# Optimization experiments

Measured on AMD Instinct MI355X. Metric: run time of the kernel, lower is better.

Reference implementation:

```python
import jax, jax.numpy as jnp
import numpy as np

R = 512   # rnn_size
K = 2     # context_size (number of memories in queue)


def _lstm_cell(x, h, c, Wih, Whh, bih, bhh):
    # PyTorch LSTMCell: gates ordered i, f, g, o
    gates = x @ Wih.T + h @ Whh.T + bih + bhh
    i, f, g, o = jnp.split(gates, 4, axis=1)
    i = jax.nn.sigmoid(i)
    f = jax.nn.sigmoid(f)
    g = jnp.tanh(g)
    o = jax.nn.sigmoid(o)
    c = f * c + i * g
    h = o * jnp.tanh(c)
    return h, c


def setup_inputs() -> dict:
    key = jax.random.key(0)
    ks = jax.random.split(key, 12)
    T, B, N = 64, 16, 256
    emb_utts = jax.random.normal(ks[0], (T, B, R), jnp.float32)
    M = jax.random.normal(ks[1], (K, B, N, R), jnp.float32)
    z = jnp.zeros((B, R), jnp.float32)
    s = 0.1  # param init scale to avoid gate saturation
    params = {
        'Wih_r': s * jax.random.normal(ks[2], (4 * R, 2 * R), jnp.float32),
        'Whh_r': s * jax.random.normal(ks[3], (4 * R, R), jnp.float32),
        'bih_r': s * jax.random.normal(ks[4], (4 * R,), jnp.float32),
        'bhh_r': s * jax.random.normal(ks[5], (4 * R,), jnp.float32),
        'Wc':    s * jax.random.normal(ks[6], (R, K * R + R), jnp.float32),
        'bc':    s * jax.random.normal(ks[7], (R,), jnp.float32),
        'Wih_w': s * jax.random.normal(ks[8], (4 * R, R), jnp.float32),
        'Whh_w': s * jax.random.normal(ks[9], (4 * R, R), jnp.float32),
        'bih_w': s * jax.random.normal(ks[10], (4 * R,), jnp.float32),
        'bhh_w': s * jax.random.normal(ks[11], (4 * R,), jnp.float32),
    }
    return dict(emb_utts=emb_utts, hr0=z, cr0=z, hw0=z, cw0=z,
                init_output=z, M=M, **params)


def reference(emb_utts, hr0, cr0, hw0, cw0, init_output, M,
              Wih_r, Whh_r, bih_r, bhh_r, Wc, bc,
              Wih_w, Whh_w, bih_w, bhh_w):
    B = emb_utts.shape[1]

    def step(carry, w):
        hr, cr, hw, cw, Mq = carry
        # input_feed: out is never updated in the original loop -> init_output
        x = jnp.concatenate([w, init_output], axis=1)
        hr, cr = _lstm_cell(x, hr, cr, Wih_r, Whh_r, bih_r, bhh_r)
        # read each memory: sim [K,B,N], z softmax over slots, m [K,B,R]
        sim = jnp.einsum('br,kbnr->kbn', hr, Mq)
        z = jax.nn.softmax(sim, axis=-1)
        m = jnp.einsum('kbn,kbnr->kbr', z, Mq)
        cattet = jnp.concatenate(
            [hr, m.transpose(1, 0, 2).reshape(B, K * R)], axis=1)
        comp = jax.nn.softmax(cattet @ Wc.T + bc, axis=-1)
        hw, cw = _lstm_cell(comp, hw, cw, Wih_w, Whh_w, bih_w, bhh_w)
        # NTM-style update: M_new = (1 - z) * (M + hw)
        erase = 1.0 - z[..., None]                    # [K,B,N,1]
        Mq = erase * (Mq + hw[None, :, None, :])      # [K,B,N,R]
        return (hr, cr, hw, cw, Mq), hw

    (hr, cr, hw, cw, Mf), outputs = jax.lax.scan(
        step, (hr0, cr0, hw0, cw0, M), emb_utts)
    return outputs, hr, cr, hw, cw, Mf
```

## Files before the change

### kernel.cpp

```cpp
#include <hip/hip_runtime.h>
#include <math.h>

#define RR 512
#define BB 16
#define TT 64
#define KC 2
#define NN 256
#define NBLK 256

__device__ __forceinline__ float sigmoidf_(float x) {
    return 1.0f / (1.0f + __expf(-x));
}
__device__ __forceinline__ float wave_sum(float v) {
    #pragma unroll
    for (int off = 32; off > 0; off >>= 1) v += __shfl_xor(v, off, 64);
    return v;
}
__device__ __forceinline__ float wave_max(float v) {
    #pragma unroll
    for (int off = 32; off > 0; off >>= 1) v = fmaxf(v, __shfl_xor(v, off, 64));
    return v;
}

__device__ __forceinline__ float ldA(const float* p) {
    return __hip_atomic_load(p, __ATOMIC_RELAXED, __HIP_MEMORY_SCOPE_AGENT);
}
__device__ __forceinline__ void stA(float* p, float v) {
    __hip_atomic_store(p, v, __ATOMIC_RELAXED, __HIP_MEMORY_SCOPE_AGENT);
}
__device__ __forceinline__ unsigned ldU(const unsigned* p) {
    return __hip_atomic_load(p, __ATOMIC_RELAXED, __HIP_MEMORY_SCOPE_AGENT);
}
__device__ __forceinline__ void stU(unsigned* p, unsigned v) {
    __hip_atomic_store(p, v, __ATOMIC_RELAXED, __HIP_MEMORY_SCOPE_AGENT);
}
__device__ __forceinline__ float2 ldA2(const float* p) {
    unsigned long long v = __hip_atomic_load((const unsigned long long*)p,
                                             __ATOMIC_RELAXED, __HIP_MEMORY_SCOPE_AGENT);
    float2 r;
    r.x = __uint_as_float((unsigned)v);
    r.y = __uint_as_float((unsigned)(v >> 32));
    return r;
}
__device__ __forceinline__ void stA2(float* p, float x, float y) {
    unsigned long long v = ((unsigned long long)__float_as_uint(y) << 32)
                         | (unsigned long long)__float_as_uint(x);
    __hip_atomic_store((unsigned long long*)p, v, __ATOMIC_RELAXED,
                       __HIP_MEMORY_SCOPE_AGENT);
}


#define LDG8(d0,d1,d2,d3,d4,d5,d6,d7, q0,q1,q2,q3,q4,q5,q6,q7)      \
    asm volatile(                                                     \
        "global_load_dwordx4 %0, %8, off sc0 sc1\n\t"                \
        "global_load_dwordx4 %1, %9, off sc0 sc1\n\t"                \
        "global_load_dwordx4 %2, %10, off sc0 sc1\n\t"               \
        "global_load_dwordx4 %3, %11, off sc0 sc1\n\t"               \
        "global_load_dwordx4 %4, %12, off sc0 sc1\n\t"               \
        "global_load_dwordx4 %5, %13, off sc0 sc1\n\t"               \
        "global_load_dwordx4 %6, %14, off sc0 sc1\n\t"               \
        "global_load_dwordx4 %7, %15, off sc0 sc1\n\t"               \
        "s_waitcnt vmcnt(0)"                                          \
        : "=&v"(d0), "=&v"(d1), "=&v"(d2), "=&v"(d3),                 \
          "=&v"(d4), "=&v"(d5), "=&v"(d6), "=&v"(d7)                  \
        : "v"(q0), "v"(q1), "v"(q2), "v"(q3),                         \
          "v"(q4), "v"(q5), "v"(q6), "v"(q7)                          \
        : "memory")

#define LDG16O(d0,d1,d2,d3,d4,d5,d6,d7,d8,d9,d10,d11,d12,d13,d14,d15,\
               q0,q1,q2,q3)                                           \
    asm volatile(                                                     \
        "global_load_dwordx4 %0, %16, off sc0 sc1\n\t"               \
        "global_load_dwordx4 %1, %16, off offset:1024 sc0 sc1\n\t"   \
        "global_load_dwordx4 %2, %16, off offset:2048 sc0 sc1\n\t"   \
        "global_load_dwordx4 %3, %16, off offset:3072 sc0 sc1\n\t"   \
        "global_load_dwordx4 %4, %17, off sc0 sc1\n\t"               \
        "global_load_dwordx4 %5, %17, off offset:1024 sc0 sc1\n\t"   \
        "global_load_dwordx4 %6, %17, off offset:2048 sc0 sc1\n\t"   \
        "global_load_dwordx4 %7, %17, off offset:3072 sc0 sc1\n\t"   \
        "global_load_dwordx4 %8, %18, off sc0 sc1\n\t"               \
        "global_load_dwordx4 %9, %18, off offset:1024 sc0 sc1\n\t"   \
        "global_load_dwordx4 %10, %18, off offset:2048 sc0 sc1\n\t"  \
        "global_load_dwordx4 %11, %18, off offset:3072 sc0 sc1\n\t"  \
        "global_load_dwordx4 %12, %19, off sc0 sc1\n\t"              \
        "global_load_dwordx4 %13, %19, off offset:1024 sc0 sc1\n\t"  \
        "global_load_dwordx4 %14, %19, off offset:2048 sc0 sc1\n\t"  \
        "global_load_dwordx4 %15, %19, off offset:3072 sc0 sc1\n\t"  \
        "s_waitcnt vmcnt(0)"                                          \
        : "=&v"(d0), "=&v"(d1), "=&v"(d2), "=&v"(d3),                 \
          "=&v"(d4), "=&v"(d5), "=&v"(d6), "=&v"(d7),                 \
          "=&v"(d8), "=&v"(d9), "=&v"(d10), "=&v"(d11),               \
          "=&v"(d12), "=&v"(d13), "=&v"(d14), "=&v"(d15)              \
        : "v"(q0), "v"(q1), "v"(q2), "v"(q3)                          \
        : "memory")

struct f8 { float4 a, b; };
__device__ __forceinline__ f8 ld8s(const float* row, int lane) {
    f8 r;
    r.a = *(const float4*)(row + lane * 4);
    r.b = *(const float4*)(row + 256 + lane * 4);
    return r;
}
__device__ __forceinline__ void st8s(float* row, const f8& v, int lane) {
    *(float4*)(row + lane * 4) = v.a;
    *(float4*)(row + 256 + lane * 4) = v.b;
}
__device__ __forceinline__ f8 ld8sA2(const float* row, int lane) {
    float2 t0 = ldA2(row + lane * 4);
    float2 t1 = ldA2(row + lane * 4 + 2);
    float2 t2 = ldA2(row + 256 + lane * 4);
    float2 t3 = ldA2(row + 256 + lane * 4 + 2);
    f8 r;
    r.a = make_float4(t0.x, t0.y, t1.x, t1.y);
    r.b = make_float4(t2.x, t2.y, t3.x, t3.y);
    return r;
}
__device__ __forceinline__ float dot8(const f8& x, const f8& y) {
    return x.a.x*y.a.x + x.a.y*y.a.y + x.a.z*y.a.z + x.a.w*y.a.w
         + x.b.x*y.b.x + x.b.y*y.b.y + x.b.z*y.b.z + x.b.w*y.b.w;
}
__device__ __forceinline__ void upd8(f8& m, const f8& u, float zf) {
    m.a.x = zf * (m.a.x + u.a.x); m.a.y = zf * (m.a.y + u.a.y);
    m.a.z = zf * (m.a.z + u.a.z); m.a.w = zf * (m.a.w + u.a.w);
    m.b.x = zf * (m.b.x + u.b.x); m.b.y = zf * (m.b.y + u.b.y);
    m.b.z = zf * (m.b.z + u.b.z); m.b.w = zf * (m.b.w + u.b.w);
}
__device__ __forceinline__ void fmaacc8(f8& acc, float sc, const f8& m, float wgt) {
    acc.a.x = acc.a.x*sc + wgt*m.a.x; acc.a.y = acc.a.y*sc + wgt*m.a.y;
    acc.a.z = acc.a.z*sc + wgt*m.a.z; acc.a.w = acc.a.w*sc + wgt*m.a.w;
    acc.b.x = acc.b.x*sc + wgt*m.b.x; acc.b.y = acc.b.y*sc + wgt*m.b.y;
    acc.b.z = acc.b.z*sc + wgt*m.b.z; acc.b.w = acc.b.w*sc + wgt*m.b.w;
}

__device__ __forceinline__ float reduce16(float* p, int lane) {
    float q[8];
    {
        bool hi = (lane & 32) != 0;
        #pragma unroll
        for (int i = 0; i < 8; ++i) {
            float snd = hi ? p[i] : p[i + 8];
            float r = __shfl_xor(snd, 32, 64);
            q[i] = (hi ? p[i + 8] : p[i]) + r;
        }
    }
    float s4[4];
    {
        bool hi = (lane & 16) != 0;
        #pragma unroll
        for (int i = 0; i < 4; ++i) {
            float snd = hi ? q[i] : q[i + 4];
            float r = __shfl_xor(snd, 16, 64);
            s4[i] = (hi ? q[i + 4] : q[i]) + r;
        }
    }
    float d2[2];
    {
        bool hi = (lane & 8) != 0;
        #pragma unroll
        for (int i = 0; i < 2; ++i) {
            float snd = hi ? s4[i] : s4[i + 2];
            float r = __shfl_xor(snd, 8, 64);
            d2[i] = (hi ? s4[i + 2] : s4[i]) + r;
        }
    }
    float v;
    {
        bool hi = (lane & 4) != 0;
        float snd = hi ? d2[0] : d2[1];
        float r = __shfl_xor(snd, 4, 64);
        v = (hi ? d2[1] : d2[0]) + r;
    }
    v += __shfl_xor(v, 2, 64);
    v += __shfl_xor(v, 1, 64);
    return v;
}

__device__ __forceinline__ float gatedotR(const f8* A, const f8& w, int lane) {
    float p[16];
    #pragma unroll
    for (int b = 0; b < 16; ++b) p[b] = dot8(A[b], w);
    return reduce16(p, lane);
}
__device__ __forceinline__ float gatedotL(const float* act, const f8& w, int lane) {
    float p[16];
    #pragma unroll
    for (int b = 0; b < 16; ++b) {
        f8 r = ld8s(act + b * 512, lane);
        p[b] = dot8(r, w);
    }
    return reduce16(p, lane);
}
__device__ __forceinline__ void ldacts(f8* A, const float* act, int lane) {
    #pragma unroll
    for (int b = 0; b < 16; ++b) A[b] = ld8s(act + b * 512, lane);
}

__device__ __forceinline__ void barArrive(unsigned* slots, int sidx, unsigned tgt) {
    asm volatile("s_waitcnt vmcnt(0)" ::: "memory");
    __syncthreads();
    if (threadIdx.x == 0) stU(slots + sidx, tgt);
}
__device__ __forceinline__ void gridWait(unsigned* slots, unsigned tgt) {
    if (threadIdx.x < 64) {
        const unsigned* base = slots + threadIdx.x * 4;
        for (;;) {
            bool ok = (ldU(base + 0) >= tgt) & (ldU(base + 1) >= tgt)
                    & (ldU(base + 2) >= tgt) & (ldU(base + 3) >= tgt);
            if (__all(ok)) break;
            __builtin_amdgcn_s_sleep(1);
        }
    }
    __syncthreads();
}
__device__ __forceinline__ void groupWait(unsigned* slots, int gbase, unsigned tgt) {
    if (threadIdx.x < 64) {
        const unsigned* ps = slots + gbase + (threadIdx.x & 7);
        for (;;) {
            bool ok = ldU(ps) >= tgt;
            if (__all(ok)) break;
            __builtin_amdgcn_s_sleep(1);
        }
    }
    __syncthreads();
}

__global__ void k_pre(const float* __restrict__ emb, const float* __restrict__ io,
                      const float* __restrict__ Wih, const float* __restrict__ bih,
                      const float* __restrict__ bhh, float* __restrict__ pre)
{
    __shared__ float As[16][65];
    __shared__ float Bs[16][65];
    int tid = threadIdx.x;
    int row0 = blockIdx.y * 64;
    int col0 = blockIdx.x * 64;
    int ty = tid >> 4, tx = tid & 15;
    float acc[4][4] = {};
    int lr = tid >> 2;
    int lk4 = (tid & 3) * 4;
    for (int k0 = 0; k0 < 1024; k0 += 16) {
        int grow = row0 + lr;
        int b = grow & 15;
        #pragma unroll
        for (int q = 0; q < 4; ++q) {
            int k = k0 + lk4 + q;
            float v = (k < RR) ? emb[(size_t)grow * RR + k]
                               : io[(size_t)b * RR + (k - RR)];
            As[lk4 + q][lr] = v;
        }
        #pragma unroll
        for (int q = 0; q < 4; ++q) {
            int k = k0 + lk4 + q;
            Bs[lk4 + q][lr] = Wih[(size_t)(col0 + lr) * 1024 + k];
        }
        __syncthreads();
        #pragma unroll
        for (int kk = 0; kk < 16; ++kk) {
            float a[4], bbv[4];
            #pragma unroll
            for (int i = 0; i < 4; ++i) a[i] = As[kk][ty * 4 + i];
            #pragma unroll
            for (int j = 0; j < 4; ++j) bbv[j] = Bs[kk][tx * 4 + j];
            #pragma unroll
            for (int i = 0; i < 4; ++i)
                #pragma unroll
                for (int j = 0; j < 4; ++j)
                    acc[i][j] += a[i] * bbv[j];
        }
        __syncthreads();
    }
    #pragma unroll
    for (int i = 0; i < 4; ++i) {
        int grow = row0 + ty * 4 + i;
        #pragma unroll
        for (int j = 0; j < 4; ++j) {
            int gcol = col0 + tx * 4 + j;
            pre[(size_t)grow * 2048 + gcol] = acc[i][j] + bih[gcol] + bhh[gcol];
        }
    }
}

struct P {
    const float *pre, *Whh_r, *Wc, *bc, *Wih_w, *Whh_w, *bih_w, *bhh_w;
    const float *hr0, *cr0, *hw0, *cw0, *M0;
    float *mbuf, *comppre, *mpart, *mxpart, *sumpart;
    float *hrb0, *hrb1, *crS, *hwb0, *hwb1, *cwS;
    float *outputs, *Mw;
    unsigned *slots;
};

__global__ void __launch_bounds__(256, 1) k_persist(P p)
{
    const int tid = threadIdx.x;
    const int bid = blockIdx.x;
    const int wv = tid >> 6;
    const int lane = tid & 63;
    const int u0 = bid * 2;
    const int kb = (bid & 7) * 4 + (bid >> 6);
    const int w2 = (bid >> 3) & 7;
    const int bM = kb & 15;
    const int rowG = kb * 256 + w2 * 32;
    const int sidx = kb * 8 + w2;
    const int gbase = kb * 8;

    __shared__ float Mlds[32][512];
    __shared__ float actH[16 * 512];
    __shared__ float actW[16 * 512];
    __shared__ float smacc[4][512];
    __shared__ float smx4[4], ssh4[4];
    __shared__ float simL[32];
    __shared__ float gsm[2][4][16];
    __shared__ float cc[2][2][16];
    __shared__ float wmx[16][2], wsm[16][2];
    __shared__ float bcsh[2];

    unsigned tg = 0;
    float mxK = 0.f, sumInvK = 0.f;
    float crR = 0.f, cwR = 0.f;

    const int jA = wv * 512 + u0;
    const f8 wR0 = ld8s(p.Whh_r + (size_t)jA * 512, lane);
    const f8 wR1 = ld8s(p.Whh_r + (size_t)(jA + 1) * 512, lane);
    const f8 wW0 = ld8s(p.Whh_w + (size_t)jA * 512, lane);
    const f8 wW1 = ld8s(p.Whh_w + (size_t)(jA + 1) * 512, lane);
    const f8 wI0 = ld8s(p.Wih_w + (size_t)jA * 512, lane);
    const f8 wI1 = ld8s(p.Wih_w + (size_t)(jA + 1) * 512, lane);
    const float bw0 = p.bih_w[jA] + p.bhh_w[jA];
    const float bw1 = p.bih_w[jA + 1] + p.bhh_w[jA + 1];
    const int jj = wv >> 1, part = wv & 1;
    const int jC = u0 + jj;
    f8 wC0, wC1 = {};
    if (part == 0) {
        wC0 = ld8s(p.Wc + (size_t)jC * 1536, lane);
        wC1 = ld8s(p.Wc + (size_t)jC * 1536 + 512, lane);
    } else {
        wC0 = ld8s(p.Wc + (size_t)jC * 1536 + 1024, lane);
    }
    if (tid < 2) bcsh[tid] = p.bc[u0 + tid];
    if (tid < 32) cwR = p.cw0[(tid & 15) * 512 + u0 + (tid >> 4)];

    {
        const float4* src = (const float4*)(p.M0 + (size_t)rowG * 512);
        float4* dst = (float4*)&Mlds[0][0];
        #pragma unroll 4
        for (int idx = tid; idx < 32 * 128; idx += 256)
            dst[idx] = src[idx];
    }

    {
        f8 A[16]; ldacts(A, p.hr0, lane);
        float gv0 = gatedotR(A, wR0, lane);
        float gv1 = gatedotR(A, wR1, lane);
        if ((lane & 3) == 0) {
            int b = (lane >> 2) & 15;
            gsm[0][wv][b] = gv0 + p.pre[(size_t)b * 2048 + jA];
            gsm[1][wv][b] = gv1 + p.pre[(size_t)b * 2048 + jA + 1];
        }
        __syncthreads();
        if (tid < 32) {
            int b = tid & 15, uu = tid >> 4;
            int u = u0 + uu;
            float gi = sigmoidf_(gsm[uu][0][b]);
            float gf = sigmoidf_(gsm[uu][1][b]);
            float gg = tanhf(gsm[uu][2][b]);
            float go = sigmoidf_(gsm[uu][3][b]);
            float c = gf * p.cr0[b * 512 + u] + gi * gg;
            crR = c;
            stA(p.hrb0 + b * 512 + u, go * tanhf(c));
        }
        ++tg; barArrive(p.slots, sidx, tg); gridWait(p.slots, tg);
    }

    for (int t = 0; t < TT; ++t) {
        const float* hrcur  = (t & 1) ? p.hrb1 : p.hrb0;
        float*       hrnext = (t & 1) ? p.hrb0 : p.hrb1;
        const float* hwprev = (t == 0) ? p.hw0 : (((t - 1) & 1) ? p.hwb1 : p.hwb0);
        float*       hwnext = (t & 1) ? p.hwb1 : p.hwb0;

        {
            float4 ha[8], wa[8];
            const float* hsrc = hrcur + tid * 4;
            const float* wsrc = hwprev + tid * 4;
            LDG8(ha[0], ha[1], ha[2], ha[3], ha[4], ha[5], ha[6], ha[7],
                 hsrc, hsrc + 1024, hsrc + 2048, hsrc + 3072,
                 hsrc + 4096, hsrc + 5120, hsrc + 6144, hsrc + 7168);
            LDG8(wa[0], wa[1], wa[2], wa[3], wa[4], wa[5], wa[6], wa[7],
                 wsrc, wsrc + 1024, wsrc + 2048, wsrc + 3072,
                 wsrc + 4096, wsrc + 5120, wsrc + 6144, wsrc + 7168);
            #pragma unroll
            for (int q = 0; q < 8; ++q) {
                ((float4*)actH)[q * 256 + tid] = ha[q];
                ((float4*)actW)[q * 256 + tid] = wa[q];
            }
        }
        __syncthreads();

        {
            f8 h = ld8s(actH + bM * 512, lane);
            f8 w8 = {};
            if (t > 0) w8 = ld8s(actW + bM * 512, lane);
            float mx = -3.0e38f, ssum = 0.f;
            f8 macc = {};
            #pragma unroll
            for (int ii = 0; ii < 8; ++ii) {
                int rl = wv * 8 + ii;
                float4* mp0 = (float4*)&Mlds[rl][lane * 4];
                float4* mp1 = (float4*)&Mlds[rl][256 + lane * 4];
                f8 m; m.a = *mp0; m.b = *mp1;
                if (t > 0) {
                    float zf = 1.0f - __expf(simL[rl] - mxK) * sumInvK;
                    upd8(m, w8, zf);
                    *mp0 = m.a; *mp1 = m.b;
                }
                float s = wave_sum(dot8(m, h));
                float nmx = fmaxf(mx, s);
                float sc = __expf(mx - nmx);
                float wgt = __expf(s - nmx);
                fmaacc8(macc, sc, m, wgt);
                ssum = ssum * sc + wgt;
                mx = nmx;
                if (lane == 0) simL[rl] = s;
            }
            if (lane == 0) { smx4[wv] = mx; ssh4[wv] = ssum; }
            __syncthreads();
            float MXb = fmaxf(fmaxf(smx4[0], smx4[1]), fmaxf(smx4[2], smx4[3]));
            float sc2 = __expf(mx - MXb);
            float* d0 = &smacc[wv][lane * 4];
            float* d1 = &smacc[wv][256 + lane * 4];
            d0[0] = macc.a.x * sc2; d0[1] = macc.a.y * sc2;
            d0[2] = macc.a.z * sc2; d0[3] = macc.a.w * sc2;
            d1[0] = macc.b.x * sc2; d1[1] = macc.b.y * sc2;
            d1[2] = macc.b.z * sc2; d1[3] = macc.b.w * sc2;
            __syncthreads();
            {
                int r2 = tid * 2;
                float s0 = smacc[0][r2] + smacc[1][r2] + smacc[2][r2] + smacc[3][r2];
                float s1 = smacc[0][r2 + 1] + smacc[1][r2 + 1]
                         + smacc[2][r2 + 1] + smacc[3][r2 + 1];
                stA2(&p.mpart[(size_t)(kb * 8 + w2) * 512 + r2], s0, s1);
            }
            if (tid == 0) {
                float sB = ssh4[0] * __expf(smx4[0] - MXb)
                         + ssh4[1] * __expf(smx4[1] - MXb)
                         + ssh4[2] * __expf(smx4[2] - MXb)
                         + ssh4[3] * __expf(smx4[3] - MXb);
                stA(&p.mxpart[kb * 8 + w2], MXb);
                stA(&p.sumpart[kb * 8 + w2], sB);
            }
        }
        if (t < 63) {
            float gv0 = gatedotL(actH, wR0, lane);
            float gv1 = gatedotL(actH, wR1, lane);
            if ((lane & 3) == 0) {
                int b = (lane >> 2) & 15;
                gsm[0][wv][b] = gv0 + p.pre[(size_t)((t + 1) * 16 + b) * 2048 + jA];
                gsm[1][wv][b] = gv1 + p.pre[(size_t)((t + 1) * 16 + b) * 2048 + jA + 1];
            }
            __syncthreads();
            if (tid < 32) {
                int b = tid & 15, uu = tid >> 4;
                int u = u0 + uu;
                float gi = sigmoidf_(gsm[uu][0][b]);
                float gf = sigmoidf_(gsm[uu][1][b]);
                float gg = tanhf(gsm[uu][2][b]);
                float go = sigmoidf_(gsm[uu][3][b]);
                float c = gf * crR + gi * gg;
                crR = c;
                stA(hrnext + b * 512 + u, go * tanhf(c));
            }
        }

        ++tg; barArrive(p.slots, sidx, tg); groupWait(p.slots, gbase, tg);
        {
            float mxp[8];
            #pragma unroll
            for (int w3 = 0; w3 < 8; ++w3) mxp[w3] = ldA(&p.mxpart[kb * 8 + w3]);
            float MX = -3.0e38f;
            #pragma unroll
            for (int w3 = 0; w3 < 8; ++w3) MX = fmaxf(MX, mxp[w3]);
            float SUM = 0.f;
            #pragma unroll
            for (int w3 = 0; w3 < 8; ++w3)
                SUM += ldA(&p.sumpart[kb * 8 + w3]) * __expf(mxp[w3] - MX);
            mxK = MX;
            sumInvK = 1.0f / SUM;
            if (tid < 32) {
                int r2 = w2 * 64 + tid * 2;
                float a0 = 0.f, a1 = 0.f;
                #pragma unroll
                for (int w3 = 0; w3 < 8; ++w3) {
                    float cf = __expf(mxp[w3] - MX);
                    float2 v2 = ldA2(&p.mpart[(size_t)(kb * 8 + w3) * 512 + r2]);
                    a0 += cf * v2.x;
                    a1 += cf * v2.y;
                }
                stA2(&p.mbuf[(size_t)kb * 512 + r2], a0 * sumInvK, a1 * sumInvK);
            }
        }
        ++tg; barArrive(p.slots, sidx, tg); gridWait(p.slots, tg);

        float vh0, vh1;
        {
            vh0 = gatedotL(actW, wW0, lane);
            vh1 = gatedotL(actW, wW1, lane);
        }
        {
            float v;
            f8 Am[16];
            const float* msbase = p.mbuf + (part ? 16 * 512 : 0) + lane * 4;
            LDG16O(Am[0].a, Am[0].b, Am[1].a, Am[1].b,
                   Am[2].a, Am[2].b, Am[3].a, Am[3].b,
                   Am[4].a, Am[4].b, Am[5].a, Am[5].b,
                   Am[6].a, Am[6].b, Am[7].a, Am[7].b,
                   msbase, msbase + 1024, msbase + 2048, msbase + 3072);
            LDG16O(Am[8].a, Am[8].b, Am[9].a, Am[9].b,
                   Am[10].a, Am[10].b, Am[11].a, Am[11].b,
                   Am[12].a, Am[12].b, Am[13].a, Am[13].b,
                   Am[14].a, Am[14].b, Am[15].a, Am[15].b,
                   msbase + 4096, msbase + 5120, msbase + 6144, msbase + 7168);
            if (part == 0) {
                v = gatedotL(actH, wC0, lane) + gatedotR(Am, wC1, lane);
            } else {
                v = gatedotR(Am, wC0, lane);
            }
            if ((lane & 3) == 0) {
                int b = (lane >> 2) & 15;
                cc[jj][part][b] = v;
            }
            __syncthreads();
            if (tid < 32) {
                int b = tid & 15, jj2 = tid >> 4;
                stA(&p.comppre[b * 512 + (u0 + jj2)],
                    cc[jj2][0][b] + cc[jj2][1][b] + bcsh[jj2]);
            }
        }
        ++tg; barArrive(p.slots, sidx, tg); gridWait(p.slots, tg);

        {
            float4 v4[8];
            const float* cs = p.comppre + tid * 4;
            LDG8(v4[0], v4[1], v4[2], v4[3], v4[4], v4[5], v4[6], v4[7],
                 cs, cs + 1024, cs + 2048, cs + 3072,
                 cs + 4096, cs + 5120, cs + 6144, cs + 7168);
            const int bpar = wv >> 1;
            #pragma unroll
            for (int k = 0; k < 8; ++k) {
                float mk = fmaxf(fmaxf(v4[k].x, v4[k].y), fmaxf(v4[k].z, v4[k].w));
                mk = wave_max(mk);
                if (lane == 0) wmx[2 * k + bpar][wv & 1] = mk;
            }
            __syncthreads();
            float4* Eld4 = (float4*)actH;
            #pragma unroll
            for (int k = 0; k < 8; ++k) {
                float mxb = fmaxf(wmx[2 * k + bpar][0], wmx[2 * k + bpar][1]);
                float e0 = __expf(v4[k].x - mxb), e1 = __expf(v4[k].y - mxb);
                float e2 = __expf(v4[k].z - mxb), e3 = __expf(v4[k].w - mxb);
                Eld4[k * 256 + tid] = make_float4(e0, e1, e2, e3);
                float sv = wave_sum(e0 + e1 + e2 + e3);
                if (lane == 0) wsm[2 * k + bpar][wv & 1] = sv;
            }
            __syncthreads();
            float ti0 = gatedotL(actH, wI0, lane);
            float ti1 = gatedotL(actH, wI1, lane);
            if ((lane & 3) == 0) {
                int bb = (lane >> 2) & 15;
                float siv = 1.0f / (wsm[bb][0] + wsm[bb][1]);
                gsm[0][wv][bb] = ti0 * siv + vh0 + bw0;
                gsm[1][wv][bb] = ti1 * siv + vh1 + bw1;
            }
            __syncthreads();
            if (tid < 32) {
                int bb = tid & 15, uu = tid >> 4;
                int u = u0 + uu;
                float gi = sigmoidf_(gsm[uu][0][bb]);
                float gf = sigmoidf_(gsm[uu][1][bb]);
                float gg = tanhf(gsm[uu][2][bb]);
                float go = sigmoidf_(gsm[uu][3][bb]);
                float c = gf * cwR + gi * gg;
                cwR = c;
                float h = go * tanhf(c);
                stA(hwnext + bb * 512 + u, h);
                p.outputs[(size_t)t * 8192 + bb * 512 + u] = h;
            }
        }
        ++tg; barArrive(p.slots, sidx, tg); gridWait(p.slots, tg);
    }

    {
        f8 w8 = ld8sA2(p.hwb1 + (size_t)bM * 512, lane);
        #pragma unroll
        for (int ii = 0; ii < 8; ++ii) {
            int rl = wv * 8 + ii;
            float zf = 1.0f - __expf(simL[rl] - mxK) * sumInvK;
            f8 m;
            m.a = *(float4*)&Mlds[rl][lane * 4];
            m.b = *(float4*)&Mlds[rl][256 + lane * 4];
            upd8(m, w8, zf);
            st8s(p.Mw + (size_t)(rowG + rl) * 512, m, lane);
        }
        if (tid < 32) {
            int b = tid & 15, uu = tid >> 4;
            int u = u0 + uu;
            p.crS[b * 512 + u] = crR;
            p.cwS[b * 512 + u] = cwR;
        }
    }
}

extern "C" void kernel_launch(void* const* d_in, const int* in_sizes, int n_in,
                              void* d_out, int out_size, void* d_ws, size_t ws_size,
                              hipStream_t stream) {
    const float* emb   = (const float*)d_in[0];
    const float* hr0   = (const float*)d_in[1];
    const float* cr0   = (const float*)d_in[2];
    const float* hw0   = (const float*)d_in[3];
    const float* cw0   = (const float*)d_in[4];
    const float* io    = (const float*)d_in[5];
    const float* M0    = (const float*)d_in[6];
    const float* Wih_r = (const float*)d_in[7];
    const float* bih_r = (const float*)d_in[9];
    const float* bhh_r = (const float*)d_in[10];

    float* out = (float*)d_out;
    float* outputs = out;
    float* hrS1 = out + 524288;
    float* crS  = out + 532480;
    float* hwS1 = out + 540672;
    float* cwS  = out + 548864;
    float* Mw   = out + 557056;

    float* ws = (float*)d_ws;
    float* pre     = ws;
    float* mbuf    = ws + 2097152;
    float* comppre = mbuf + 16384;
    float* hrB0    = comppre + 8192;
    float* hwB0    = hrB0 + 8192;
    float* mpart   = hwB0 + 8192;
    float* mxpart  = mpart + 131072;
    float* sumpart = mxpart + 256;
    unsigned* slots = (unsigned*)(sumpart + 256);

    (void)hipMemsetAsync(slots, 0, 256 * sizeof(unsigned), stream);

    k_pre<<<dim3(32, 16), 256, 0, stream>>>(emb, io, Wih_r, bih_r, bhh_r, pre);

    P p;
    p.pre = pre;
    p.Whh_r = (const float*)d_in[8];
    p.Wc    = (const float*)d_in[11];
    p.bc    = (const float*)d_in[12];
    p.Wih_w = (const float*)d_in[13];
    p.Whh_w = (const float*)d_in[14];
    p.bih_w = (const float*)d_in[15];
    p.bhh_w = (const float*)d_in[16];
    p.hr0 = hr0; p.cr0 = cr0; p.hw0 = hw0; p.cw0 = cw0; p.M0 = M0;
    p.mbuf = mbuf; p.comppre = comppre;
    p.mpart = mpart; p.mxpart = mxpart; p.sumpart = sumpart;
    p.hrb0 = hrB0; p.hrb1 = hrS1; p.crS = crS;
    p.hwb0 = hwB0; p.hwb1 = hwS1; p.cwS = cwS;
    p.outputs = outputs; p.Mw = Mw;
    p.slots = slots;

    k_persist<<<NBLK, 256, 0, stream>>>(p);
}
```

Baseline: 1.964 ms.

## Double block size to 512 threads, one gate row per wave

Launches the persistent kernel with 8 waves per block instead of 4. Each wave now owns a single gate row for the recurrent, write and input dot products, and handles half as many memory rows in the read and update phase. The composition dot products are spread over six waves, and the staging loads and softmax reductions are re-indexed to match. The aim is to shorten each serial step between grid barriers by spreading the work over more waves, at the cost of more register pressure per block, wider LDS reductions and extra idle threads in some phases.

```diff
diff --git a/kernel.cpp b/kernel.cpp
--- a/kernel.cpp
+++ b/kernel.cpp
@@ -48,7 +48,6 @@
     __hip_atomic_store((unsigned long long*)p, v, __ATOMIC_RELAXED,
                        __HIP_MEMORY_SCOPE_AGENT);
 }
-
 
 #define LDG8(d0,d1,d2,d3,d4,d5,d6,d7, q0,q1,q2,q3,q4,q5,q6,q7)      \
     asm volatile(                                                     \
@@ -65,6 +64,17 @@
           "=&v"(d4), "=&v"(d5), "=&v"(d6), "=&v"(d7)                  \
         : "v"(q0), "v"(q1), "v"(q2), "v"(q3),                         \
           "v"(q4), "v"(q5), "v"(q6), "v"(q7)                          \
+        : "memory")
+
+#define LDG4(d0,d1,d2,d3, q0,q1,q2,q3)                                \
+    asm volatile(                                                     \
+        "global_load_dwordx4 %0, %4, off sc0 sc1\n\t"                \
+        "global_load_dwordx4 %1, %5, off sc0 sc1\n\t"                \
+        "global_load_dwordx4 %2, %6, off sc0 sc1\n\t"                \
+        "global_load_dwordx4 %3, %7, off sc0 sc1\n\t"                \
+        "s_waitcnt vmcnt(0)"                                          \
+        : "=&v"(d0), "=&v"(d1), "=&v"(d2), "=&v"(d3)                  \
+        : "v"(q0), "v"(q1), "v"(q2), "v"(q3)                          \
         : "memory")
 
 #define LDG16O(d0,d1,d2,d3,d4,d5,d6,d7,d8,d9,d10,d11,d12,d13,d14,d15,\
@@ -288,7 +298,7 @@
     unsigned *slots;
 };
 
-__global__ void __launch_bounds__(256, 1) k_persist(P p)
+__global__ void __launch_bounds__(512, 1) k_persist(P p)
 {
     const int tid = threadIdx.x;
     const int bid = blockIdx.x;
@@ -302,14 +312,17 @@
     const int sidx = kb * 8 + w2;
     const int gbase = kb * 8;
 
+    const int gateW = wv >> 1, uuW = wv & 1;
+    const int jAw = gateW * 512 + u0 + uuW;
+
     __shared__ float Mlds[32][512];
-    __shared__ float actH[16 * 512];
-    __shared__ float actW[16 * 512];
-    __shared__ float smacc[4][512];
-    __shared__ float smx4[4], ssh4[4];
+    __shared__ float bufH[16 * 512];
+    __shared__ float bufW[16 * 512];
+    __shared__ float smacc[8][512];
+    __shared__ float smx8[8], ssh8[8];
     __shared__ float simL[32];
     __shared__ float gsm[2][4][16];
-    __shared__ float cc[2][2][16];
+    __shared__ float cc[2][3][16];
     __shared__ float wmx[16][2], wsm[16][2];
     __shared__ float bcsh[2];
 
@@ -317,43 +330,32 @@
     float mxK = 0.f, sumInvK = 0.f;
     float crR = 0.f, cwR = 0.f;
 
-    const int jA = wv * 512 + u0;
-    const f8 wR0 = ld8s(p.Whh_r + (size_t)jA * 512, lane);
-    const f8 wR1 = ld8s(p.Whh_r + (size_t)(jA + 1) * 512, lane);
-    const f8 wW0 = ld8s(p.Whh_w + (size_t)jA * 512, lane);
-    const f8 wW1 = ld8s(p.Whh_w + (size_t)(jA + 1) * 512, lane);
-    const f8 wI0 = ld8s(p.Wih_w + (size_t)jA * 512, lane);
-    const f8 wI1 = ld8s(p.Wih_w + (size_t)(jA + 1) * 512, lane);
-    const float bw0 = p.bih_w[jA] + p.bhh_w[jA];
-    const float bw1 = p.bih_w[jA + 1] + p.bhh_w[jA + 1];
-    const int jj = wv >> 1, part = wv & 1;
-    const int jC = u0 + jj;
-    f8 wC0, wC1 = {};
-    if (part == 0) {
-        wC0 = ld8s(p.Wc + (size_t)jC * 1536, lane);
-        wC1 = ld8s(p.Wc + (size_t)jC * 1536 + 512, lane);
-    } else {
-        wC0 = ld8s(p.Wc + (size_t)jC * 1536 + 1024, lane);
-    }
+    const f8 wRj = ld8s(p.Whh_r + (size_t)jAw * 512, lane);
+    const f8 wWj = ld8s(p.Whh_w + (size_t)jAw * 512, lane);
+    const f8 wIj = ld8s(p.Wih_w + (size_t)jAw * 512, lane);
+    const float bwj = p.bih_w[jAw] + p.bhh_w[jAw];
+    const int jjC = (wv < 2) ? wv : ((wv < 4) ? wv - 2 : wv - 4);
+    const int itmC = (wv < 2) ? 0 : ((wv < 4) ? 1 : 2);
+    f8 wCj = {};
+    if (wv < 6)
+        wCj = ld8s(p.Wc + (size_t)(u0 + jjC) * 1536 + itmC * 512, lane);
     if (tid < 2) bcsh[tid] = p.bc[u0 + tid];
     if (tid < 32) cwR = p.cw0[(tid & 15) * 512 + u0 + (tid >> 4)];
 
     {
         const float4* src = (const float4*)(p.M0 + (size_t)rowG * 512);
         float4* dst = (float4*)&Mlds[0][0];
-        #pragma unroll 4
-        for (int idx = tid; idx < 32 * 128; idx += 256)
+        #pragma unroll 2
+        for (int idx = tid; idx < 32 * 128; idx += 512)
             dst[idx] = src[idx];
     }
 
     {
         f8 A[16]; ldacts(A, p.hr0, lane);
-        float gv0 = gatedotR(A, wR0, lane);
-        float gv1 = gatedotR(A, wR1, lane);
+        float gv = gatedotR(A, wRj, lane);
         if ((lane & 3) == 0) {
             int b = (lane >> 2) & 15;
-            gsm[0][wv][b] = gv0 + p.pre[(size_t)b * 2048 + jA];
-            gsm[1][wv][b] = gv1 + p.pre[(size_t)b * 2048 + jA + 1];
+            gsm[uuW][gateW][b] = gv + p.pre[(size_t)b * 2048 + jAw];
         }
         __syncthreads();
         if (tid < 32) {
@@ -377,32 +379,29 @@
         float*       hwnext = (t & 1) ? p.hwb1 : p.hwb0;
 
         {
-            float4 ha[8], wa[8];
-            const float* hsrc = hrcur + tid * 4;
-            const float* wsrc = hwprev + tid * 4;
-            LDG8(ha[0], ha[1], ha[2], ha[3], ha[4], ha[5], ha[6], ha[7],
-                 hsrc, hsrc + 1024, hsrc + 2048, hsrc + 3072,
-                 hsrc + 4096, hsrc + 5120, hsrc + 6144, hsrc + 7168);
-            LDG8(wa[0], wa[1], wa[2], wa[3], wa[4], wa[5], wa[6], wa[7],
-                 wsrc, wsrc + 1024, wsrc + 2048, wsrc + 3072,
-                 wsrc + 4096, wsrc + 5120, wsrc + 6144, wsrc + 7168);
-            #pragma unroll
-            for (int q = 0; q < 8; ++q) {
-                ((float4*)actH)[q * 256 + tid] = ha[q];
-                ((float4*)actW)[q * 256 + tid] = wa[q];
+            float4 st[8];
+            const float* h0 = hrcur + tid * 4;
+            const float* g0 = hwprev + tid * 4;
+            LDG8(st[0], st[1], st[2], st[3], st[4], st[5], st[6], st[7],
+                 h0, h0 + 2048, h0 + 4096, h0 + 6144,
+                 g0, g0 + 2048, g0 + 4096, g0 + 6144);
+            #pragma unroll
+            for (int q = 0; q < 4; ++q) {
+                ((float4*)bufH)[q * 512 + tid] = st[q];
+                ((float4*)bufW)[q * 512 + tid] = st[4 + q];
             }
         }
         __syncthreads();
 
         {
-            f8 h = ld8s(actH + bM * 512, lane);
+            f8 h = ld8s(bufH + bM * 512, lane);
             f8 w8 = {};
-            if (t > 0) w8 = ld8s(actW + bM * 512, lane);
+            if (t > 0) w8 = ld8s(bufW + bM * 512, lane);
             float mx = -3.0e38f, ssum = 0.f;
             f8 macc = {};
             #pragma unroll
-            for (int ii = 0; ii < 8; ++ii) {
-                int rl = wv * 8 + ii;
+            for (int ii = 0; ii < 4; ++ii) {
+                int rl = wv * 4 + ii;
                 float4* mp0 = (float4*)&Mlds[rl][lane * 4];
                 float4* mp1 = (float4*)&Mlds[rl][256 + lane * 4];
                 f8 m; m.a = *mp0; m.b = *mp1;
@@ -420,9 +419,11 @@
                 mx = nmx;
                 if (lane == 0) simL[rl] = s;
             }
-            if (lane == 0) { smx4[wv] = mx; ssh4[wv] = ssum; }
+            if (lane == 0) { smx8[wv] = mx; ssh8[wv] = ssum; }
             __syncthreads();
-            float MXb = fmaxf(fmaxf(smx4[0], smx4[1]), fmaxf(smx4[2], smx4[3]));
+            float MXb = smx8[0];
+            #pragma unroll
+            for (int w3 = 1; w3 < 8; ++w3) MXb = fmaxf(MXb, smx8[w3]);
             float sc2 = __expf(mx - MXb);
             float* d0 = &smacc[wv][lane * 4];
             float* d1 = &smacc[wv][256 + lane * 4];
@@ -431,29 +432,30 @@
             d1[0] = macc.b.x * sc2; d1[1] = macc.b.y * sc2;
             d1[2] = macc.b.z * sc2; d1[3] = macc.b.w * sc2;
             __syncthreads();
-            {
+            if (tid < 256) {
                 int r2 = tid * 2;
-                float s0 = smacc[0][r2] + smacc[1][r2] + smacc[2][r2] + smacc[3][r2];
-                float s1 = smacc[0][r2 + 1] + smacc[1][r2 + 1]
-                         + smacc[2][r2 + 1] + smacc[3][r2 + 1];
+                float s0 = 0.f, s1 = 0.f;
+                #pragma unroll
+                for (int w3 = 0; w3 < 8; ++w3) {
+                    s0 += smacc[w3][r2];
+                    s1 += smacc[w3][r2 + 1];
+                }
                 stA2(&p.mpart[(size_t)(kb * 8 + w2) * 512 + r2], s0, s1);
             }
             if (tid == 0) {
-                float sB = ssh4[0] * __expf(smx4[0] - MXb)
-                         + ssh4[1] * __expf(smx4[1] - MXb)
-                         + ssh4[2] * __expf(smx4[2] - MXb)
-                         + ssh4[3] * __expf(smx4[3] - MXb);
+                float sB = 0.f;
+                #pragma unroll
+                for (int w3 = 0; w3 < 8; ++w3)
+                    sB += ssh8[w3] * __expf(smx8[w3] - MXb);
                 stA(&p.mxpart[kb * 8 + w2], MXb);
                 stA(&p.sumpart[kb * 8 + w2], sB);
             }
         }
         if (t < 63) {
-            float gv0 = gatedotL(actH, wR0, lane);
-            float gv1 = gatedotL(actH, wR1, lane);
+            float gv = gatedotL(bufH, wRj, lane);
             if ((lane & 3) == 0) {
                 int b = (lane >> 2) & 15;
-                gsm[0][wv][b] = gv0 + p.pre[(size_t)((t + 1) * 16 + b) * 2048 + jA];
-                gsm[1][wv][b] = gv1 + p.pre[(size_t)((t + 1) * 16 + b) * 2048 + jA + 1];
+                gsm[uuW][gateW][b] = gv + p.pre[(size_t)((t + 1) * 16 + b) * 2048 + jAw];
             }
             __syncthreads();
             if (tid < 32) {
@@ -498,75 +500,66 @@
         }
         ++tg; barArrive(p.slots, sidx, tg); gridWait(p.slots, tg);
 
-        float vh0, vh1;
+        float vhJ = gatedotL(bufW, wWj, lane);
         {
-            vh0 = gatedotL(actW, wW0, lane);
-            vh1 = gatedotL(actW, wW1, lane);
-        }
-        {
-            float v;
-            f8 Am[16];
-            const float* msbase = p.mbuf + (part ? 16 * 512 : 0) + lane * 4;
-            LDG16O(Am[0].a, Am[0].b, Am[1].a, Am[1].b,
-                   Am[2].a, Am[2].b, Am[3].a, Am[3].b,
-                   Am[4].a, Am[4].b, Am[5].a, Am[5].b,
-                   Am[6].a, Am[6].b, Am[7].a, Am[7].b,
-                   msbase, msbase + 1024, msbase + 2048, msbase + 3072);
-            LDG16O(Am[8].a, Am[8].b, Am[9].a, Am[9].b,
-                   Am[10].a, Am[10].b, Am[11].a, Am[11].b,
-                   Am[12].a, Am[12].b, Am[13].a, Am[13].b,
-                   Am[14].a, Am[14].b, Am[15].a, Am[15].b,
-                   msbase + 4096, msbase + 5120, msbase + 6144, msbase + 7168);
-            if (part == 0) {
-                v = gatedotL(actH, wC0, lane) + gatedotR(Am, wC1, lane);
-            } else {
-                v = gatedotR(Am, wC0, lane);
-            }
-            if ((lane & 3) == 0) {
-                int b = (lane >> 2) & 15;
-                cc[jj][part][b] = v;
+            if (wv < 2) {
+                float v = gatedotL(bufH, wCj, lane);
+                if ((lane & 3) == 0) cc[jjC][0][(lane >> 2) & 15] = v;
+            } else if (wv < 6) {
+                f8 Am[16];
+                const float* msbase = p.mbuf + (itmC - 1) * 16 * 512 + lane * 4;
+                LDG16O(Am[0].a, Am[0].b, Am[1].a, Am[1].b,
+                       Am[2].a, Am[2].b, Am[3].a, Am[3].b,
+                       Am[4].a, Am[4].b, Am[5].a, Am[5].b,
+                       Am[6].a, Am[6].b, Am[7].a, Am[7].b,
+                       msbase, msbase + 1024, msbase + 2048, msbase + 3072);
+                LDG16O(Am[8].a, Am[8].b, Am[9].a, Am[9].b,
+                       Am[10].a, Am[10].b, Am[11].a, Am[11].b,
+                       Am[12].a, Am[12].b, Am[13].a, Am[13].b,
+                       Am[14].a, Am[14].b, Am[15].a, Am[15].b,
+                       msbase + 4096, msbase + 5120, msbase + 6144, msbase + 7168);
+                float v = gatedotR(Am, wCj, lane);
+                if ((lane & 3) == 0) cc[jjC][itmC][(lane >> 2) & 15] = v;
             }
             __syncthreads();
             if (tid < 32) {
                 int b = tid & 15, jj2 = tid >> 4;
                 stA(&p.comppre[b * 512 + (u0 + jj2)],
-                    cc[jj2][0][b] + cc[jj2][1][b] + bcsh[jj2]);
+                    cc[jj2][0][b] + cc[jj2][1][b] + cc[jj2][2][b] + bcsh[jj2]);
             }
         }
         ++tg; barArrive(p.slots, sidx, tg); gridWait(p.slots, tg);
 
         {
-            float4 v4[8];
+            float4 v4[4];
             const float* cs = p.comppre + tid * 4;
-            LDG8(v4[0], v4[1], v4[2], v4[3], v4[4], v4[5], v4[6], v4[7],
-                 cs, cs + 1024, cs + 2048, cs + 3072,
-                 cs + 4096, cs + 5120, cs + 6144, cs + 7168);
-            const int bpar = wv >> 1;
-            #pragma unroll
-            for (int k = 0; k < 8; ++k) {
+            LDG4(v4[0], v4[1], v4[2], v4[3],
+                 cs, cs + 2048, cs + 4096, cs + 6144);
+            const int bhalf = wv & 1, brow = wv >> 1;
+            #pragma unroll
+            for (int k = 0; k < 4; ++k) {
                 float mk = fmaxf(fmaxf(v4[k].x, v4[k].y), fmaxf(v4[k].z, v4[k].w));
                 mk = wave_max(mk);
-                if (lane == 0) wmx[2 * k + bpar][wv & 1] = mk;
+                if (lane == 0) wmx[k * 4 + brow][bhalf] = mk;
             }
             __syncthreads();
-            float4* Eld4 = (float4*)actH;
-            #pragma unroll
-            for (int k = 0; k < 8; ++k) {
-                float mxb = fmaxf(wmx[2 * k + bpar][0], wmx[2 * k + bpar][1]);
+            float4* Eld4 = (float4*)bufH;
+            #pragma unroll
+            for (int k = 0; k < 4; ++k) {
+                int b = k * 4 + brow;
+                float mxb = fmaxf(wmx[b][0], wmx[b][1]);
                 float e0 = __expf(v4[k].x - mxb), e1 = __expf(v4[k].y - mxb);
                 float e2 = __expf(v4[k].z - mxb), e3 = __expf(v4[k].w - mxb);
-                Eld4[k * 256 + tid] = make_float4(e0, e1, e2, e3);
+                Eld4[k * 512 + tid] = make_float4(e0, e1, e2, e3);
                 float sv = wave_sum(e0 + e1 + e2 + e3);
-                if (lane == 0) wsm[2 * k + bpar][wv & 1] = sv;
+                if (lane == 0) wsm[b][bhalf] = sv;
             }
             __syncthreads();
-            float ti0 = gatedotL(actH, wI0, lane);
-            float ti1 = gatedotL(actH, wI1, lane);
+            float ti = gatedotL(bufH, wIj, lane);
             if ((lane & 3) == 0) {
                 int bb = (lane >> 2) & 15;
                 float siv = 1.0f / (wsm[bb][0] + wsm[bb][1]);
-                gsm[0][wv][bb] = ti0 * siv + vh0 + bw0;
-                gsm[1][wv][bb] = ti1 * siv + vh1 + bw1;
+                gsm[uuW][gateW][bb] = ti * siv + vhJ + bwj;
             }
             __syncthreads();
             if (tid < 32) {
@@ -589,8 +582,8 @@
     {
         f8 w8 = ld8sA2(p.hwb1 + (size_t)bM * 512, lane);
         #pragma unroll
-        for (int ii = 0; ii < 8; ++ii) {
-            int rl = wv * 8 + ii;
+        for (int ii = 0; ii < 4; ++ii) {
+            int rl = wv * 4 + ii;
             float zf = 1.0f - __expf(simL[rl] - mxK) * sumInvK;
             f8 m;
             m.a = *(float4*)&Mlds[rl][lane * 4];
@@ -661,5 +654,5 @@
     p.outputs = outputs; p.Mw = Mw;
     p.slots = slots;
 
-    k_persist<<<NBLK, 256, 0, stream>>>(p);
-}
+    k_persist<<<NBLK, 512, 0, stream>>>(p);
+}
```

After: 1.646 ms. 1.19x faster.
